# Performance work log

Hardware: AMD Instinct MI355X
Metric: run time of the kernel (lower is better)

## Reference

```python
import jax, jax.numpy as jnp
import numpy as np

NUM_HEADS = 8
LN_EPS = 1e-5

def _ln(x, g, b):
    mu = jnp.mean(x, axis=-1, keepdims=True)
    var = jnp.mean((x - mu) ** 2, axis=-1, keepdims=True)
    return (x - mu) * jax.lax.rsqrt(var + LN_EPS) * g + b

def _rel_index(H, W):
    coords = np.stack(np.meshgrid(np.arange(H), np.arange(W), indexing='ij'))  # (2,H,W)
    cf = coords.reshape(2, -1)
    rel = (cf[:, :, None] - cf[:, None, :]).transpose(1, 2, 0)  # (N,N,2)
    rel = rel + np.array([H - 1, W - 1])
    rel[..., 0] *= 2 * W - 1
    return rel.sum(-1)  # (N,N) int

def _biases(H, W):
    bh = np.arange(1 - H, H)
    bw = np.arange(1 - W, W)
    b = np.stack(np.meshgrid(bh, bw, indexing='ij')).reshape(2, -1).T
    return b.astype(np.float32)  # ((2H-1)*(2W-1), 2)

def setup_inputs() -> dict:
    key = jax.random.key(0)
    ks = jax.random.split(key, 8)
    dim, heads, pd = 256, NUM_HEADS, 16
    B, H, W = 256, 16, 16
    s = lambda k, shp, fan: jax.random.normal(k, shp, jnp.float32) * (fan ** -0.5)
    return {
        'x': jax.random.normal(ks[0], (B, dim, H, W), jnp.float32),
        'qkv_w': s(ks[1], (3 * dim, dim), dim), 'qkv_b': jnp.zeros((3 * dim,), jnp.float32),
        'proj_w': s(ks[2], (dim, dim), dim), 'proj_b': jnp.zeros((dim,), jnp.float32),
        'pos_proj_w': s(ks[3], (pd, 2), 2), 'pos_proj_b': jnp.zeros((pd,), jnp.float32),
        'ln1_g': jnp.ones((pd,), jnp.float32), 'ln1_b': jnp.zeros((pd,), jnp.float32),
        'fc1_w': s(ks[4], (pd, pd), pd), 'fc1_b': jnp.zeros((pd,), jnp.float32),
        'ln2_g': jnp.ones((pd,), jnp.float32), 'ln2_b': jnp.zeros((pd,), jnp.float32),
        'fc2_w': s(ks[5], (pd, pd), pd), 'fc2_b': jnp.zeros((pd,), jnp.float32),
        'ln3_g': jnp.ones((pd,), jnp.float32), 'ln3_b': jnp.zeros((pd,), jnp.float32),
        'fc3_w': s(ks[6], (heads, pd), pd), 'fc3_b': jnp.zeros((heads,), jnp.float32),
    }

def reference(x, qkv_w, qkv_b, proj_w, proj_b, pos_proj_w, pos_proj_b,
              ln1_g, ln1_b, fc1_w, fc1_b, ln2_g, ln2_b, fc2_w, fc2_b,
              ln3_g, ln3_b, fc3_w, fc3_b):
    B, C, H, W = x.shape
    N, h = H * W, NUM_HEADS
    d = C // h
    scale = d ** -0.5
    xt = x.reshape(B, C, N).transpose(0, 2, 1)  # (B,N,C)
    qkv = (jnp.einsum('bnc,oc->bno', xt, qkv_w) + qkv_b)
    qkv = qkv.reshape(B, N, 3, h, d).transpose(2, 0, 3, 1, 4)  # (3,B,h,N,d)
    q, k, v = qkv[0] * scale, qkv[1], qkv[2]
    attn = jnp.einsum('bhnd,bhmd->bhnm', q, k)  # (B,h,N,N)
    # dynamic position bias MLP over ((2H-1)(2W-1), 2) offsets
    biases = jnp.asarray(_biases(H, W))
    p = biases @ pos_proj_w.T + pos_proj_b
    p = jax.nn.relu(_ln(p, ln1_g, ln1_b)) @ fc1_w.T + fc1_b
    p = jax.nn.relu(_ln(p, ln2_g, ln2_b)) @ fc2_w.T + fc2_b
    p = jax.nn.relu(_ln(p, ln3_g, ln3_b)) @ fc3_w.T + fc3_b  # (L, h)
    idx = jnp.asarray(_rel_index(H, W))  # (N,N)
    rpb = p[idx].transpose(2, 0, 1)  # (h,N,N)
    attn = jax.nn.softmax(attn + rpb[None], axis=-1)
    out = jnp.einsum('bhnm,bhmd->bhnd', attn, v).transpose(0, 2, 1, 3).reshape(B, N, C)
    out = jnp.einsum('bnc,oc->bno', out, proj_w) + proj_b
    return out.transpose(0, 2, 1).reshape(B, C, H, W)
```

## Files before the change

kernel.cpp:

```cpp
#include <hip/hip_runtime.h>

typedef __bf16 bf16;
typedef __bf16 bf16x8 __attribute__((ext_vector_type(8)));
typedef __bf16 bf16x4 __attribute__((ext_vector_type(4)));
typedef float f32x4 __attribute__((ext_vector_type(4)));
typedef float f32x16 __attribute__((ext_vector_type(16)));
typedef unsigned int u32;
typedef unsigned int u32x2 __attribute__((ext_vector_type(2)));
typedef unsigned int u32x4 __attribute__((ext_vector_type(4)));

#define MFMA16(a, b, c) __builtin_amdgcn_mfma_f32_16x16x32_bf16(a, b, c, 0, 0, 0)
#define MFMA32(a, b, c) __builtin_amdgcn_mfma_f32_32x32x16_bf16(a, b, c, 0, 0, 0)

__device__ __forceinline__ u32 pack2(float a, float b) {
  unsigned short ua = __builtin_bit_cast(unsigned short, (bf16)a);
  unsigned short ub = __builtin_bit_cast(unsigned short, (bf16)b);
  return (u32)ua | ((u32)ub << 16);
}

__device__ __forceinline__ void lnrelu16(const float* in, float* out,
                                         const float* __restrict__ g,
                                         const float* __restrict__ b) {
  float mu = 0.f;
#pragma unroll
  for (int t = 0; t < 16; ++t) mu += in[t];
  mu *= 0.0625f;
  float var = 0.f;
#pragma unroll
  for (int t = 0; t < 16; ++t) { float d = in[t] - mu; var += d * d; }
  var *= 0.0625f;
  float inv = rsqrtf(var + 1e-5f);
#pragma unroll
  for (int t = 0; t < 16; ++t) {
    float v = (in[t] - mu) * inv * g[t] + b[t];
    out[t] = fmaxf(v, 0.f);
  }
}

__global__ __launch_bounds__(256) void k_prep(
    const float* __restrict__ qkvw, bf16* __restrict__ wqkv,
    const float* __restrict__ pjw, bf16* __restrict__ wpj,
    const float* __restrict__ ppw, const float* __restrict__ ppb,
    const float* __restrict__ g1, const float* __restrict__ b1,
    const float* __restrict__ f1w, const float* __restrict__ f1b,
    const float* __restrict__ g2, const float* __restrict__ b2,
    const float* __restrict__ f2w, const float* __restrict__ f2b,
    const float* __restrict__ g3, const float* __restrict__ b3,
    const float* __restrict__ f3w, const float* __restrict__ f3b,
    float* __restrict__ ptab) {
  const int blk = blockIdx.x;
  if (blk < 96) {
    int t = blk * 256 + threadIdx.x;
    int lane = t & 63, fk = t >> 6;
    int ot = fk >> 3, kc = fk & 7;
    int o = ot * 16 + (lane & 15), cb = kc * 32 + (lane >> 4) * 8;
    const float* src = qkvw + o * 256 + cb;
    bf16x8 v;
#pragma unroll
    for (int j = 0; j < 8; ++j) v[j] = (bf16)src[j];
    *(bf16x8*)(wqkv + (size_t)t * 8) = v;
  } else if (blk < 160) {
    int i = (blk - 96) * 256 + threadIdx.x;
    if (i < 16384) {
      float4 v = ((const float4*)pjw)[i];
      bf16x4 o;
      o[0] = (bf16)v.x; o[1] = (bf16)v.y; o[2] = (bf16)v.z; o[3] = (bf16)v.w;
      ((bf16x4*)wpj)[i] = o;
    }
  } else {
    int l = (blk - 160) * 256 + threadIdx.x;
    if (l >= 961) return;
    float dh = (float)(l / 31) - 15.f;
    float dw = (float)(l % 31) - 15.f;
    float p[16], a[16], y[16];
#pragma unroll
    for (int t = 0; t < 16; ++t)
      p[t] = dh * ppw[2 * t] + dw * ppw[2 * t + 1] + ppb[t];
    lnrelu16(p, a, g1, b1);
#pragma unroll
    for (int t = 0; t < 16; ++t) {
      float s = f1b[t];
#pragma unroll
      for (int u = 0; u < 16; ++u) s += a[u] * f1w[t * 16 + u];
      y[t] = s;
    }
    lnrelu16(y, a, g2, b2);
#pragma unroll
    for (int t = 0; t < 16; ++t) {
      float s = f2b[t];
#pragma unroll
      for (int u = 0; u < 16; ++u) s += a[u] * f2w[t * 16 + u];
      p[t] = s;
    }
    lnrelu16(p, a, g3, b3);
#pragma unroll
    for (int t = 0; t < 8; ++t) {
      float s = f3b[t];
#pragma unroll
      for (int u = 0; u < 16; ++u) s += a[u] * f3w[t * 16 + u];
      ptab[l * 8 + t] = s;
    }
  }
}

__global__ __launch_bounds__(256) void k_bias(const float* __restrict__ ptab,
                                              bf16* __restrict__ Bsw) {
  int idx = blockIdx.x * 256 + threadIdx.x;
  int lane = idx & 63, tg = idx >> 6;
  int h = tg >> 6, qt = (tg >> 3) & 7, kt2 = tg & 7;
  int l31 = lane & 31, hi2 = lane >> 5;
  int n = qt * 32 + l31;
  int i1 = n >> 4, j1 = n & 15;
  bf16x8 o0, o1;
#pragma unroll
  for (int reg = 0; reg < 16; ++reg) {
    int key = kt2 * 32 + (reg & 3) + 8 * (reg >> 2) + 4 * hi2;
    int i2 = key >> 4, j2 = key & 15;
    int li = (i1 - i2 + 15) * 31 + (j1 - j2 + 15);
    bf16 v = (bf16)ptab[li * 8 + h];
    if (reg < 8) o0[reg] = v; else o1[reg - 8] = v;
  }
  bf16* dst = Bsw + tg * 1024 + lane * 16;
  *(bf16x8*)dst = o0;
  *(bf16x8*)(dst + 8) = o1;
}

__global__ __launch_bounds__(512) void k_qkv(
    const float* __restrict__ x, const bf16* __restrict__ Wf,
    const float* __restrict__ qb, bf16* __restrict__ q, bf16* __restrict__ kk,
    bf16* __restrict__ vT) {
  __shared__ bf16 Xl[128 * 256];
  __shared__ bf16 Vb[8][16 * 36];
  const int b = blockIdx.x >> 1;
  const int nh = blockIdx.x & 1;
  const int tid = threadIdx.x;
  const int lane = tid & 63;
  const int wave = tid >> 6;
  const int wm = wave & 1, wo = wave >> 1;
  const int l15 = lane & 15, l4 = lane >> 4;
  const int n0w = nh * 128 + wm * 64;

  {
    const float* xb = x + b * 65536 + nh * 128;
    const int p = tid & 3;
    const int Q = tid >> 2;
    const int n0 = (Q & 31) * 4;
    const int cgb = Q >> 5;
    float4 vv[16];
#pragma unroll
    for (int it = 0; it < 16; ++it) {
      const int c0 = (cgb + it * 4) * 4;
      vv[it] = *(const float4*)(xb + (c0 + p) * 256 + n0);
    }
#pragma unroll
    for (int it = 0; it < 16; ++it) {
      const int c0 = (cgb + it * 4) * 4;
      float4 v = vv[it];
      u32 u0 = pack2(v.x, v.y);
      u32 u1 = pack2(v.z, v.w);
      u32 su0 = __shfl_xor(u0, 1);
      u32 su1 = __shfl_xor(u1, 1);
      u32 w, z;
      if (p & 1) {
        w = (su0 >> 16) | (u0 & 0xffff0000u);
        z = (su1 >> 16) | (u1 & 0xffff0000u);
      } else {
        w = (u0 & 0xffffu) | (su0 << 16);
        z = (u1 & 0xffffu) | (su1 << 16);
      }
      u32 sw = __shfl_xor(w, 2);
      u32 sz = __shfl_xor(z, 2);
      u32x2 o2;
      o2[0] = (p & 2) ? sz : w;
      o2[1] = (p & 2) ? z : sw;
      const int n = n0 + p;
      const int wb = (2 * c0) ^ ((n & 7) << 4);
      *(u32x2*)((char*)Xl + n * 512 + wb) = o2;
    }
  }
  __syncthreads();

  const f32x4 fz = {0.f, 0.f, 0.f, 0.f};
  bf16* lb = Vb[wave];
  for (int og = 0; og < 3; ++og) {
    const int ot0 = wo * 12 + og * 4;
    f32x4 acc[4][4];
#pragma unroll
    for (int nt = 0; nt < 4; ++nt)
#pragma unroll
      for (int oi = 0; oi < 4; ++oi) acc[nt][oi] = fz;

    bf16x8 afr[2][4], bfr[2][4];
#pragma unroll
    for (int nt = 0; nt < 4; ++nt) {
      int nn = wm * 64 + nt * 16 + l15;
      int wb = (l4 * 16) ^ ((nn & 7) << 4);
      afr[0][nt] = *(const bf16x8*)((const char*)Xl + nn * 512 + wb);
    }
#pragma unroll
    for (int oi = 0; oi < 4; ++oi)
      bfr[0][oi] = *(const bf16x8*)(Wf + (((ot0 + oi) * 8) * 64 + lane) * 8);

#pragma unroll
    for (int kc = 0; kc < 8; ++kc) {
      const int cur = kc & 1, nxt = cur ^ 1;
      if (kc < 7) {
#pragma unroll
        for (int nt = 0; nt < 4; ++nt) {
          int nn = wm * 64 + nt * 16 + l15;
          int wb = ((kc + 1) * 64 + l4 * 16) ^ ((nn & 7) << 4);
          afr[nxt][nt] = *(const bf16x8*)((const char*)Xl + nn * 512 + wb);
        }
#pragma unroll
        for (int oi = 0; oi < 4; ++oi)
          bfr[nxt][oi] =
              *(const bf16x8*)(Wf + ((((ot0 + oi) * 8) + kc + 1) * 64 + lane) * 8);
      }
#pragma unroll
      for (int nt = 0; nt < 4; ++nt)
#pragma unroll
        for (int oi = 0; oi < 4; ++oi)
          acc[nt][oi] = MFMA16(afr[cur][nt], bfr[cur][oi], acc[nt][oi]);
    }

    const int seg = ot0 >> 4;
    if (seg < 2) {
      bf16* dstbuf = (seg == 0) ? q : kk;
      const float scale = (seg == 0) ? 0.17677669529663687f : 1.0f;
#pragma unroll
      for (int p = 0; p < 2; ++p) {
        int ot = ot0 + 2 * p;
        int h = (ot >> 1) & 7;
        int base = (b * 8 + h) * 8192;
        float bias0 = qb[seg * 256 + h * 32 + l15];
        float bias1 = qb[seg * 256 + h * 32 + 16 + l15];
#pragma unroll
        for (int nt = 0; nt < 4; ++nt) {
#pragma unroll
          for (int r = 0; r < 4; ++r) {
            int row = l4 * 4 + r;
            lb[row * 36 + l15] = (bf16)((acc[nt][2 * p][r] + bias0) * scale);
            lb[row * 36 + 16 + l15] =
                (bf16)((acc[nt][2 * p + 1][r] + bias1) * scale);
          }
          asm volatile("s_waitcnt lgkmcnt(0)" ::: "memory");
          __builtin_amdgcn_sched_barrier(0);
          int row = lane >> 2, ch = lane & 3;
          bf16x8 tv = *(const bf16x8*)(lb + row * 36 + ch * 8);
          asm volatile("s_waitcnt lgkmcnt(0)" ::: "memory");
          __builtin_amdgcn_sched_barrier(0);
          *(bf16x8*)(dstbuf + base + (n0w + nt * 16 + row) * 32 + ch * 8) = tv;
        }
      }
    } else {
#pragma unroll
      for (int oi = 0; oi < 4; ++oi) {
        int ot = ot0 + oi;
        int o = ot * 16 + l15;
        float bias = qb[o];
        int h = (o >> 5) & 7;
        int d = o & 31;
        int base = (b * 8 + h) * 8192;
#pragma unroll
        for (int pr = 0; pr < 2; ++pr) {
          f32x4 acc0 = acc[2 * pr][oi], acc1 = acc[2 * pr + 1][oi];
          int n0p = n0w + pr * 32;
#pragma unroll
          for (int nt = 0; nt < 2; ++nt) {
            f32x4 a = nt ? acc1 : acc0;
            *(u32*)(lb + l15 * 36 + nt * 16 + l4 * 4) =
                pack2(a[0] + bias, a[1] + bias);
            *(u32*)(lb + l15 * 36 + nt * 16 + l4 * 4 + 2) =
                pack2(a[2] + bias, a[3] + bias);
          }
          asm volatile("s_waitcnt lgkmcnt(0)" ::: "memory");
          __builtin_amdgcn_sched_barrier(0);
          int dl = lane >> 2, chv = lane & 3;
          bf16x4 rv0 = *(bf16x4*)(lb + dl * 36 + chv * 8);
          bf16x4 rv1 = *(bf16x4*)(lb + dl * 36 + chv * 8 + 4);
          asm volatile("s_waitcnt lgkmcnt(0)" ::: "memory");
          __builtin_amdgcn_sched_barrier(0);
          int d2 = (ot & 1) * 16 + dl;
          bf16* dv2 = vT + base + d2 * 256 + n0p + chv * 8;
          *(bf16x4*)dv2 = rv0;
          *(bf16x4*)(dv2 + 4) = rv1;
        }
      }
    }
  }
}

__global__ __launch_bounds__(256, 4) void k_attn(
    const bf16* __restrict__ q, const bf16* __restrict__ kk,
    const bf16* __restrict__ vT, const bf16* __restrict__ Bsw,
    bf16* __restrict__ ao) {
  __shared__ bf16 Kl[256 * 36];
  __shared__ bf16 Ob[4][32 * 36];
  const int bh = blockIdx.x;
  const int b = bh >> 3, h = bh & 7;
  const int tid = threadIdx.x;
  const int lane = tid & 63, wave = tid >> 6;
  const int l31 = lane & 31, hi = lane >> 5;

  const bf16* Kg = kk + bh * 8192;
#pragma unroll
  for (int i = 0; i < 4; ++i) {
    int t = tid + i * 256;
    int n = t >> 2, dc = t & 3;
    *(bf16x8*)(Kl + n * 36 + dc * 8) = *(const bf16x8*)(Kg + n * 32 + dc * 8);
  }
  __syncthreads();

  const bf16* Vg = vT + bh * 8192;
  bf16* ob = Ob[wave];
  for (int qi = 0; qi < 2; ++qi) {
    const int qt = wave * 2 + qi, q0 = qt * 32;
    bf16x8 qf0 = *(const bf16x8*)(q + bh * 8192 + (q0 + l31) * 32 + hi * 8);
    bf16x8 qf1 = *(const bf16x8*)(q + bh * 8192 + (q0 + l31) * 32 + 16 + hi * 8);
    const bf16* bq = Bsw + (h * 8 + qt) * 8192 + lane * 16;
    float lsum = 0.f;
    f32x16 o;
#pragma unroll
    for (int i = 0; i < 16; ++i) o[i] = 0.f;
#pragma unroll
    for (int kt2 = 0; kt2 < 8; ++kt2) {
      u32x4 w0 = *(const u32x4*)(bq + kt2 * 1024);
      u32x4 w1 = *(const u32x4*)(bq + kt2 * 1024 + 8);
      f32x16 acc;
#pragma unroll
      for (int j = 0; j < 4; ++j) {
        acc[2 * j] = __builtin_bit_cast(float, w0[j] << 16);
        acc[2 * j + 1] = __builtin_bit_cast(float, w0[j] & 0xffff0000u);
        acc[8 + 2 * j] = __builtin_bit_cast(float, w1[j] << 16);
        acc[8 + 2 * j + 1] = __builtin_bit_cast(float, w1[j] & 0xffff0000u);
      }
      bf16x8 kf0 = *(const bf16x8*)(Kl + (kt2 * 32 + l31) * 36 + hi * 8);
      bf16x8 kf1 = *(const bf16x8*)(Kl + (kt2 * 32 + l31) * 36 + 16 + hi * 8);
      acc = MFMA32(kf0, qf0, acc);
      acc = MFMA32(kf1, qf1, acc);
      u32 lo[4], hw[4];
#pragma unroll
      for (int qq = 0; qq < 4; ++qq) {
        float e0 = __expf(acc[4 * qq]);
        float e1 = __expf(acc[4 * qq + 1]);
        float e2 = __expf(acc[4 * qq + 2]);
        float e3 = __expf(acc[4 * qq + 3]);
        lsum += (e0 + e1) + (e2 + e3);
        lo[qq] = pack2(e0, e1);
        hw[qq] = pack2(e2, e3);
      }
#pragma unroll
      for (int sb = 0; sb < 2; ++sb) {
        u32 keep_lo = hi ? lo[2 * sb + 1] : lo[2 * sb];
        u32 keep_hi = hi ? hw[2 * sb + 1] : hw[2 * sb];
        u32 send_lo = hi ? lo[2 * sb] : lo[2 * sb + 1];
        u32 send_hi = hi ? hw[2 * sb] : hw[2 * sb + 1];
        u32 rlo = __shfl_xor(send_lo, 32);
        u32 rhi = __shfl_xor(send_hi, 32);
        u32x4 bw;
        bw[0] = hi ? rlo : keep_lo;
        bw[1] = hi ? rhi : keep_hi;
        bw[2] = hi ? keep_lo : rlo;
        bw[3] = hi ? keep_hi : rhi;
        bf16x8 pf = __builtin_bit_cast(bf16x8, bw);
        bf16x8 vf = *(const bf16x8*)(Vg + l31 * 256 + kt2 * 32 + sb * 16 + hi * 8);
        o = MFMA32(vf, pf, o);
      }
    }
    lsum += __shfl_xor(lsum, 32);
    const float inv = 1.f / lsum;
#pragma unroll
    for (int qq = 0; qq < 4; ++qq) {
      *(u32*)(ob + l31 * 36 + 8 * qq + 4 * hi) =
          pack2(o[4 * qq] * inv, o[4 * qq + 1] * inv);
      *(u32*)(ob + l31 * 36 + 8 * qq + 4 * hi + 2) =
          pack2(o[4 * qq + 2] * inv, o[4 * qq + 3] * inv);
    }
    asm volatile("s_waitcnt lgkmcnt(0)" ::: "memory");
    __builtin_amdgcn_sched_barrier(0);
    int n2 = lane >> 1, ch = lane & 1;
    bf16x4 r0 = *(bf16x4*)(ob + n2 * 36 + ch * 16);
    bf16x4 r1 = *(bf16x4*)(ob + n2 * 36 + ch * 16 + 4);
    bf16x4 r2 = *(bf16x4*)(ob + n2 * 36 + ch * 16 + 8);
    bf16x4 r3 = *(bf16x4*)(ob + n2 * 36 + ch * 16 + 12);
    asm volatile("s_waitcnt lgkmcnt(0)" ::: "memory");
    __builtin_amdgcn_sched_barrier(0);
    bf16* dst = ao + (b * 256 + q0 + n2) * 256 + h * 32 + ch * 16;
    *(bf16x4*)dst = r0;
    *(bf16x4*)(dst + 4) = r1;
    *(bf16x4*)(dst + 8) = r2;
    *(bf16x4*)(dst + 12) = r3;
  }
}

__global__ __launch_bounds__(512) void k_proj(
    const bf16* __restrict__ ao, const bf16* __restrict__ Wp,
    const float* __restrict__ pb, float* __restrict__ out) {
  __shared__ bf16 Sl[2][16 * 264];
  const int b = blockIdx.x & 255;
  const int oh = blockIdx.x >> 8;
  const int tid = threadIdx.x;
  const int lane = tid & 63, wave = tid >> 6;
  const int l15 = lane & 15, l4 = lane >> 4;
  const int ot = oh * 8 + wave;
  bf16x8 af[8];
  const bf16* wr = Wp + (ot * 16 + l15) * 256 + l4 * 8;
#pragma unroll
  for (int kc = 0; kc < 8; ++kc) af[kc] = *(const bf16x8*)(wr + kc * 32);
  float bias[4];
#pragma unroll
  for (int r = 0; r < 4; ++r) bias[r] = pb[ot * 16 + l4 * 4 + r];
  const bf16* aob = ao + b * 65536;
  float* outb = out + b * 65536 + ot * 16 * 256;
  const int sr = tid >> 5, sc = (tid & 31) * 8;

  *(bf16x8*)(Sl[0] + sr * 264 + sc) = *(const bf16x8*)(aob + sr * 256 + sc);
  __syncthreads();

  const f32x4 fz = {0.f, 0.f, 0.f, 0.f};
  for (int nt = 0; nt < 16; ++nt) {
    const int cur = nt & 1;
    if (nt < 15)
      *(bf16x8*)(Sl[cur ^ 1] + sr * 264 + sc) =
          *(const bf16x8*)(aob + ((nt + 1) * 16 + sr) * 256 + sc);
    f32x4 acc = fz;
#pragma unroll
    for (int kc = 0; kc < 8; ++kc) {
      bf16x8 bfr = *(const bf16x8*)(Sl[cur] + l15 * 264 + kc * 32 + l4 * 8);
      acc = MFMA16(af[kc], bfr, acc);
    }
#pragma unroll
    for (int r = 0; r < 4; ++r)
      outb[(l4 * 4 + r) * 256 + nt * 16 + l15] = acc[r] + bias[r];
    __syncthreads();
  }
}

extern "C" void kernel_launch(void* const* d_in, const int* in_sizes, int n_in,
                              void* d_out, int out_size, void* d_ws, size_t ws_size,
                              hipStream_t stream) {
  const float* x    = (const float*)d_in[0];
  const float* qkvw = (const float*)d_in[1];
  const float* qkvb = (const float*)d_in[2];
  const float* pjw  = (const float*)d_in[3];
  const float* pjb  = (const float*)d_in[4];
  const float* ppw  = (const float*)d_in[5];
  const float* ppb  = (const float*)d_in[6];
  const float* g1 = (const float*)d_in[7];   const float* b1 = (const float*)d_in[8];
  const float* f1w = (const float*)d_in[9];  const float* f1b = (const float*)d_in[10];
  const float* g2 = (const float*)d_in[11];  const float* b2 = (const float*)d_in[12];
  const float* f2w = (const float*)d_in[13]; const float* f2b = (const float*)d_in[14];
  const float* g3 = (const float*)d_in[15];  const float* b3 = (const float*)d_in[16];
  const float* f3w = (const float*)d_in[17]; const float* f3b = (const float*)d_in[18];
  float* out = (float*)d_out;

  bf16* wsq  = (bf16*)d_ws;
  bf16* wsk  = wsq + 16777216;
  bf16* wsv  = wsk + 16777216;
  bf16* wsao = wsv + 16777216;
  float* ptab = (float*)(wsao + 16777216);
  bf16* wqkv = (bf16*)(ptab + 8192);
  bf16* wpj  = wqkv + 196608;
  bf16* bsw  = wpj + 65536;

  hipLaunchKernelGGL(k_prep, dim3(164), dim3(256), 0, stream, qkvw, wqkv, pjw,
                     wpj, ppw, ppb, g1, b1, f1w, f1b, g2, b2, f2w, f2b, g3, b3,
                     f3w, f3b, ptab);
  hipLaunchKernelGGL(k_bias, dim3(128), dim3(256), 0, stream, ptab, bsw);
  hipLaunchKernelGGL(k_qkv, dim3(512), dim3(512), 0, stream, x, wqkv, qkvb, wsq,
                     wsk, wsv);
  hipLaunchKernelGGL(k_attn, dim3(2048), dim3(256), 0, stream, wsq, wsk, wsv,
                     bsw, wsao);
  hipLaunchKernelGGL(k_proj, dim3(512), dim3(512), 0, stream, wsao, wpj, pjb, out);
}
```

Before: 159.4 us.

## Retile QKV GEMM per wave to 128 rows by 2 output tiles, drop double buffering

Each wave now covers all 128 spatial rows of the block and two 16-wide output tiles per iteration, instead of 64 rows by four output tiles. This reads each weight fragment from global once per block rather than once per row-half wave pair, which cuts global weight traffic. The price is twice as many LDS reads of the X tile per MFMA, plus the loss of the software double-buffered prefetch of A and B fragments across k-chunks, so latency now depends on the compiler's scheduling.

```diff
diff --git a/kernel.cpp b/kernel.cpp
--- a/kernel.cpp
+++ b/kernel.cpp
@@ -136,9 +136,8 @@
   const int tid = threadIdx.x;
   const int lane = tid & 63;
   const int wave = tid >> 6;
-  const int wm = wave & 1, wo = wave >> 1;
   const int l15 = lane & 15, l4 = lane >> 4;
-  const int n0w = nh * 128 + wm * 64;
+  const int n0w = nh * 128;
 
   {
     const float* xb = x + b * 65536 + nh * 128;
@@ -183,91 +182,68 @@
   const f32x4 fz = {0.f, 0.f, 0.f, 0.f};
   bf16* lb = Vb[wave];
   for (int og = 0; og < 3; ++og) {
-    const int ot0 = wo * 12 + og * 4;
-    f32x4 acc[4][4];
-#pragma unroll
-    for (int nt = 0; nt < 4; ++nt)
-#pragma unroll
-      for (int oi = 0; oi < 4; ++oi) acc[nt][oi] = fz;
-
-    bf16x8 afr[2][4], bfr[2][4];
-#pragma unroll
-    for (int nt = 0; nt < 4; ++nt) {
-      int nn = wm * 64 + nt * 16 + l15;
-      int wb = (l4 * 16) ^ ((nn & 7) << 4);
-      afr[0][nt] = *(const bf16x8*)((const char*)Xl + nn * 512 + wb);
-    }
-#pragma unroll
-    for (int oi = 0; oi < 4; ++oi)
-      bfr[0][oi] = *(const bf16x8*)(Wf + (((ot0 + oi) * 8) * 64 + lane) * 8);
+    const int ot0 = wave * 6 + og * 2;
+    f32x4 acc[8][2];
+#pragma unroll
+    for (int nt = 0; nt < 8; ++nt)
+#pragma unroll
+      for (int oi = 0; oi < 2; ++oi) acc[nt][oi] = fz;
 
 #pragma unroll
     for (int kc = 0; kc < 8; ++kc) {
-      const int cur = kc & 1, nxt = cur ^ 1;
-      if (kc < 7) {
-#pragma unroll
-        for (int nt = 0; nt < 4; ++nt) {
-          int nn = wm * 64 + nt * 16 + l15;
-          int wb = ((kc + 1) * 64 + l4 * 16) ^ ((nn & 7) << 4);
-          afr[nxt][nt] = *(const bf16x8*)((const char*)Xl + nn * 512 + wb);
-        }
-#pragma unroll
-        for (int oi = 0; oi < 4; ++oi)
-          bfr[nxt][oi] =
-              *(const bf16x8*)(Wf + ((((ot0 + oi) * 8) + kc + 1) * 64 + lane) * 8);
-      }
-#pragma unroll
-      for (int nt = 0; nt < 4; ++nt)
-#pragma unroll
-        for (int oi = 0; oi < 4; ++oi)
-          acc[nt][oi] = MFMA16(afr[cur][nt], bfr[cur][oi], acc[nt][oi]);
+      bf16x8 afr[8], bfr[2];
+#pragma unroll
+      for (int nt = 0; nt < 8; ++nt) {
+        int nn = nt * 16 + l15;
+        int wb = (kc * 64 + l4 * 16) ^ ((nn & 7) << 4);
+        afr[nt] = *(const bf16x8*)((const char*)Xl + nn * 512 + wb);
+      }
+#pragma unroll
+      for (int oi = 0; oi < 2; ++oi)
+        bfr[oi] = *(const bf16x8*)(Wf + ((((ot0 + oi) * 8) + kc) * 64 + lane) * 8);
+#pragma unroll
+      for (int nt = 0; nt < 8; ++nt)
+#pragma unroll
+        for (int oi = 0; oi < 2; ++oi)
+          acc[nt][oi] = MFMA16(afr[nt], bfr[oi], acc[nt][oi]);
     }
 
     const int seg = ot0 >> 4;
+    const int h = (ot0 >> 1) & 7;
+    const int base = (b * 8 + h) * 8192;
     if (seg < 2) {
       bf16* dstbuf = (seg == 0) ? q : kk;
       const float scale = (seg == 0) ? 0.17677669529663687f : 1.0f;
-#pragma unroll
-      for (int p = 0; p < 2; ++p) {
-        int ot = ot0 + 2 * p;
-        int h = (ot >> 1) & 7;
-        int base = (b * 8 + h) * 8192;
-        float bias0 = qb[seg * 256 + h * 32 + l15];
-        float bias1 = qb[seg * 256 + h * 32 + 16 + l15];
-#pragma unroll
-        for (int nt = 0; nt < 4; ++nt) {
-#pragma unroll
-          for (int r = 0; r < 4; ++r) {
-            int row = l4 * 4 + r;
-            lb[row * 36 + l15] = (bf16)((acc[nt][2 * p][r] + bias0) * scale);
-            lb[row * 36 + 16 + l15] =
-                (bf16)((acc[nt][2 * p + 1][r] + bias1) * scale);
-          }
-          asm volatile("s_waitcnt lgkmcnt(0)" ::: "memory");
-          __builtin_amdgcn_sched_barrier(0);
-          int row = lane >> 2, ch = lane & 3;
-          bf16x8 tv = *(const bf16x8*)(lb + row * 36 + ch * 8);
-          asm volatile("s_waitcnt lgkmcnt(0)" ::: "memory");
-          __builtin_amdgcn_sched_barrier(0);
-          *(bf16x8*)(dstbuf + base + (n0w + nt * 16 + row) * 32 + ch * 8) = tv;
+      float bias0 = qb[seg * 256 + h * 32 + l15];
+      float bias1 = qb[seg * 256 + h * 32 + 16 + l15];
+#pragma unroll
+      for (int nt = 0; nt < 8; ++nt) {
+#pragma unroll
+        for (int r = 0; r < 4; ++r) {
+          int row = l4 * 4 + r;
+          lb[row * 36 + l15] = (bf16)((acc[nt][0][r] + bias0) * scale);
+          lb[row * 36 + 16 + l15] = (bf16)((acc[nt][1][r] + bias1) * scale);
         }
+        asm volatile("s_waitcnt lgkmcnt(0)" ::: "memory");
+        __builtin_amdgcn_sched_barrier(0);
+        int row = lane >> 2, ch = lane & 3;
+        bf16x8 tv = *(const bf16x8*)(lb + row * 36 + ch * 8);
+        asm volatile("s_waitcnt lgkmcnt(0)" ::: "memory");
+        __builtin_amdgcn_sched_barrier(0);
+        *(bf16x8*)(dstbuf + base + (n0w + nt * 16 + row) * 32 + ch * 8) = tv;
       }
     } else {
 #pragma unroll
-      for (int oi = 0; oi < 4; ++oi) {
+      for (int oi = 0; oi < 2; ++oi) {
         int ot = ot0 + oi;
-        int o = ot * 16 + l15;
-        float bias = qb[o];
-        int h = (o >> 5) & 7;
-        int d = o & 31;
-        int base = (b * 8 + h) * 8192;
-#pragma unroll
-        for (int pr = 0; pr < 2; ++pr) {
-          f32x4 acc0 = acc[2 * pr][oi], acc1 = acc[2 * pr + 1][oi];
+        float bias = qb[ot * 16 + l15];
+#pragma unroll
+        for (int pr = 0; pr < 4; ++pr) {
+          f32x4 a0 = acc[2 * pr][oi], a1 = acc[2 * pr + 1][oi];
           int n0p = n0w + pr * 32;
 #pragma unroll
           for (int nt = 0; nt < 2; ++nt) {
-            f32x4 a = nt ? acc1 : acc0;
+            f32x4 a = nt ? a1 : a0;
             *(u32*)(lb + l15 * 36 + nt * 16 + l4 * 4) =
                 pack2(a[0] + bias, a[1] + bias);
             *(u32*)(lb + l15 * 36 + nt * 16 + l4 * 4 + 2) =
```

After: 156.2 us. 1.02x faster.
